# Performance work log

Measured on AMD Instinct MI355X. Metric: run time of the kernel, lower is better.

Reference implementation:

```python
import jax, jax.numpy as jnp
import numpy as np

N = 100000   # num_nodes
E = 600000   # num_edges (before self loops)
H = 128      # hidden_size
R = 16       # lora_rank
SCALING = 32.0 / 16  # lora_alpha / lora_rank
LN_EPS = 1e-5


def setup_inputs() -> dict:
    key = jax.random.key(0)
    ks = jax.random.split(key, 12)
    s = 0.02
    return {
        "hidden_states": jax.random.normal(ks[0], (N, H), dtype=jnp.float32),
        "edge_index": jax.random.randint(ks[1], (2, E), 0, N, dtype=jnp.int64),
        # message_transform (LoRALinear): base W/b + lora A/B
        "msg_W": jax.random.normal(ks[2], (H, H), dtype=jnp.float32) * s,
        "msg_b": jax.random.normal(ks[3], (H,), dtype=jnp.float32) * s,
        "msg_A": jax.random.normal(ks[4], (R, H), dtype=jnp.float32) * s,
        "msg_B": jax.random.normal(ks[5], (H, R), dtype=jnp.float32) * s,
        # gate_transform (LoRALinear)
        "gate_W": jax.random.normal(ks[6], (H, H), dtype=jnp.float32) * s,
        "gate_b": jax.random.normal(ks[7], (H,), dtype=jnp.float32) * s,
        "gate_A": jax.random.normal(ks[8], (R, H), dtype=jnp.float32) * s,
        "gate_B": jax.random.normal(ks[9], (H, R), dtype=jnp.float32) * s,
        # LayerNorm params
        "ln_gamma": jnp.ones((H,), dtype=jnp.float32),
        "ln_beta": jnp.zeros((H,), dtype=jnp.float32),
    }


def _lora_linear(x, W, b, A, B):
    # base_layer(x) + scaling * lora_B(lora_A(x)); dropout is identity at eval
    return x @ W.T + b + SCALING * ((x @ A.T) @ B.T)


def _message_passing(x, edge_index):
    n = x.shape[0]
    loops = jnp.arange(n, dtype=edge_index.dtype)
    row = jnp.concatenate([edge_index[0], loops])  # sources j
    col = jnp.concatenate([edge_index[1], loops])  # targets i
    # symmetric-ish norm: deg from targets (PyG degree(col))
    deg = jax.ops.segment_sum(jnp.ones_like(col, dtype=x.dtype), col, num_segments=n)
    dinv = jnp.where(deg > 0, deg ** -0.5, 0.0)
    norm = dinv[row] * dinv[col]                   # [E+N]
    msgs = norm[:, None] * x[row]                  # edge-gathered messages
    summed = jax.ops.segment_sum(msgs, col, num_segments=n)
    # aggr='mean': divide by per-target edge count (== deg, includes self loop)
    return summed / jnp.maximum(deg, 1.0)[:, None]


def reference(hidden_states, edge_index, msg_W, msg_b, msg_A, msg_B,
              gate_W, gate_b, gate_A, gate_B, ln_gamma, ln_beta):
    message_out = _message_passing(hidden_states, edge_index)
    message_transformed = _lora_linear(message_out, msg_W, msg_b, msg_A, msg_B)
    gate = jax.nn.sigmoid(_lora_linear(hidden_states, gate_W, gate_b, gate_A, gate_B))
    x = hidden_states + gate * message_transformed
    mu = jnp.mean(x, axis=-1, keepdims=True)
    var = jnp.mean(jnp.square(x - mu), axis=-1, keepdims=True)
    return (x - mu) / jnp.sqrt(var + LN_EPS) * ln_gamma + ln_beta
```

## Files before the change

### kernel.cpp

```cpp
#include <hip/hip_runtime.h>
#include <math.h>

#define H 128
#define RANK 16
#define SCALING 2.0f
#define LN_EPS 1e-5f
#define CHUNK 2048

typedef short bf16x8 __attribute__((ext_vector_type(8)));
typedef float f32x4 __attribute__((ext_vector_type(4)));

__device__ __forceinline__ unsigned short f2bf(float f) {
    unsigned int u = __float_as_uint(f);
    u += 0x7fffu + ((u >> 16) & 1u);
    return (unsigned short)(u >> 16);
}
__device__ __forceinline__ float bflo(unsigned int u) {
    return __uint_as_float(u << 16);
}
__device__ __forceinline__ float bfhi(unsigned int u) {
    return __uint_as_float(u & 0xffff0000u);
}

__global__ void k_init(const int* __restrict__ ei, int E, int* __restrict__ deg,
                       const float2* __restrict__ x2, int xtotal, unsigned int* __restrict__ xb,
                       const float* __restrict__ msg_W, const float* __restrict__ msg_A,
                       const float* __restrict__ msg_B,
                       const float* __restrict__ gate_W, const float* __restrict__ gate_A,
                       const float* __restrict__ gate_B,
                       unsigned short* __restrict__ Wmz, unsigned short* __restrict__ Wgz,
                       int BA, int BB) {
    int b = blockIdx.x;
    if (b < BA) {
        int e = b * 256 + threadIdx.x;
        if (e < E) atomicAdd(&deg[ei[E + e]], 1);
    } else if (b < BA + BB) {
        int idx = (b - BA) * 256 + threadIdx.x;
        if (idx < xtotal) {
            float2 v = x2[idx];
            xb[idx] = (unsigned int)f2bf(v.x) | ((unsigned int)f2bf(v.y) << 16);
        }
    } else {
        int bb = b - BA - BB;
        int which = bb >> 6;
        int idx = (bb & 63) * 256 + threadIdx.x;
        const float* W = which ? gate_W : msg_W;
        const float* A = which ? gate_A : msg_A;
        const float* Bm = which ? gate_B : msg_B;
        unsigned short* Wz = which ? Wgz : Wmz;
        int h = idx & (H - 1);
        int k = idx >> 7;
        float s = 0.f;
        #pragma unroll
        for (int r = 0; r < RANK; ++r) s = fmaf(A[r * H + k], Bm[h * RANK + r], s);
        float v = W[h * H + k] + SCALING * s;
        int kt = k >> 5, kk = k & 31, qd = kk >> 3, j = kk & 7;
        int nt = h >> 4, nl = h & 15;
        int lane = qd * 16 + nl;
        Wz[(((kt * 8 + nt) * 64 + lane) * 8) + j] = f2bf(v);
    }
}

__global__ void k_stage2(const int* __restrict__ deg, int N,
                         float* __restrict__ dinv, float* __restrict__ rdeg,
                         int* __restrict__ chunkSum, int BA) {
    int b = blockIdx.x;
    if (b < BA) {
        int i = b * 256 + threadIdx.x;
        if (i < N) {
            float d = (float)(deg[i] + 1);
            dinv[i] = rsqrtf(d);
            rdeg[i] = 1.0f / d;
        }
    } else {
        __shared__ int red[256];
        int c = b - BA;
        int base = c * CHUNK;
        int s = 0;
        for (int i = threadIdx.x; i < CHUNK; i += 256) {
            int g = base + i;
            if (g < N) s += deg[g];
        }
        red[threadIdx.x] = s;
        __syncthreads();
        for (int off = 128; off > 0; off >>= 1) {
            if (threadIdx.x < off) red[threadIdx.x] += red[threadIdx.x + off];
            __syncthreads();
        }
        if (threadIdx.x == 0) chunkSum[c] = red[0];
    }
}

__global__ void k_localscan(const int* __restrict__ deg, int N, const int* __restrict__ chunkSum,
                            int C, int* __restrict__ offsets, int* __restrict__ cursor) {
    int c = blockIdx.x, t = threadIdx.x;
    __shared__ int cbase_sh;
    __shared__ int wsum[4];
    if (t < 64) {
        int partial = 0, total = 0;
        for (int j = t; j < C; j += 64) {
            int v = chunkSum[j];
            total += v;
            if (j < c) partial += v;
        }
        #pragma unroll
        for (int off = 1; off < 64; off <<= 1) {
            partial += __shfl_xor(partial, off);
            total += __shfl_xor(total, off);
        }
        if (t == 0) {
            cbase_sh = partial;
            if (c == C - 1) offsets[N] = total;
        }
    }
    int base = c * CHUNK;
    int idx0 = base + t * 8;
    int v[8]; int tsum = 0;
    #pragma unroll
    for (int j = 0; j < 8; ++j) {
        int g = idx0 + j;
        v[j] = (g < N) ? deg[g] : 0;
        tsum += v[j];
    }
    int lane = t & 63, wv = t >> 6;
    int inc = tsum;
    #pragma unroll
    for (int off = 1; off < 64; off <<= 1) {
        int u = __shfl_up(inc, off);
        if (lane >= off) inc += u;
    }
    if (lane == 63) wsum[wv] = inc;
    __syncthreads();
    int wbase = 0;
    for (int w = 0; w < wv; ++w) wbase += wsum[w];
    int excl = wbase + inc - tsum + cbase_sh;
    #pragma unroll
    for (int j = 0; j < 8; ++j) {
        int g = idx0 + j;
        if (g < N) { offsets[g] = excl; cursor[g] = excl; excl += v[j]; }
    }
}

__global__ void k_fill(const int* __restrict__ ei, int E,
                       int* __restrict__ cursor, int* __restrict__ adj) {
    int e = blockIdx.x * blockDim.x + threadIdx.x;
    if (e < E) {
        int r = ei[e];
        int c = ei[E + e];
        int pos = atomicAdd(&cursor[c], 1);
        adj[pos] = r;
    }
}

__global__ __launch_bounds__(256) void k_gather(
    const unsigned int* __restrict__ xb, const int* __restrict__ offsets,
    const int* __restrict__ adj, const float* __restrict__ dinv,
    const float* __restrict__ rdeg, int N, unsigned int* __restrict__ msgb) {
    int wave = (blockIdx.x * 256 + threadIdx.x) >> 6;
    int lane = threadIdx.x & 63;
    if (wave >= N) return;
    int i = __builtin_amdgcn_readfirstlane(wave);
    float di = dinv[i];
    unsigned int su = xb[(size_t)i * 64 + lane];
    float ax[8], ay[8];
    ax[0] = bflo(su) * di; ay[0] = bfhi(su) * di;
    #pragma unroll
    for (int j = 1; j < 8; ++j) { ax[j] = 0.f; ay[j] = 0.f; }
    int s0 = offsets[i], s1 = offsets[i + 1];
    int last = s1 - 1;
    for (int e = s0; e < s1; e += 8) {
        int is[8]; float ws[8]; unsigned int us[8];
        #pragma unroll
        for (int j = 0; j < 8; ++j) {
            int ee = e + j;
            is[j] = __builtin_amdgcn_readfirstlane(adj[ee < s1 ? ee : last]);
        }
        #pragma unroll
        for (int j = 0; j < 8; ++j) {
            float w = dinv[is[j]];
            ws[j] = (e + j < s1) ? w : 0.f;
        }
        #pragma unroll
        for (int j = 0; j < 8; ++j) us[j] = xb[(size_t)is[j] * 64 + lane];
        #pragma unroll
        for (int j = 0; j < 8; ++j) {
            ax[j] = fmaf(ws[j], bflo(us[j]), ax[j]);
            ay[j] = fmaf(ws[j], bfhi(us[j]), ay[j]);
        }
    }
    float sc = di * rdeg[i];
    float rx = (((ax[0] + ax[1]) + (ax[2] + ax[3])) + ((ax[4] + ax[5]) + (ax[6] + ax[7]))) * sc;
    float ry = (((ay[0] + ay[1]) + (ay[2] + ay[3])) + ((ay[4] + ay[5]) + (ay[6] + ay[7]))) * sc;
    msgb[(size_t)i * 64 + lane] = (unsigned int)f2bf(rx) | ((unsigned int)f2bf(ry) << 16);
}

__global__ __launch_bounds__(256) void k_fused(
    const unsigned int* __restrict__ xb, const unsigned int* __restrict__ msgb,
    const unsigned short* __restrict__ Wmz, const unsigned short* __restrict__ Wgz,
    const float* __restrict__ msg_b, const float* __restrict__ gate_b,
    const float* __restrict__ gamma, const float* __restrict__ beta,
    float* __restrict__ out, int N) {
    int t = threadIdx.x;
    int wid = t >> 6, lane = t & 63;
    int m0 = (blockIdx.x * 4 + wid) * 16;
    if (m0 >= N) return;

    int quad = lane >> 4;
    int nl = lane & 15;

    int arow = m0 + nl; if (arow >= N) arow = N - 1;
    const bf16x8* hb8 = (const bf16x8*)xb + (size_t)arow * 16;
    const bf16x8* mb8 = (const bf16x8*)msgb + (size_t)arow * 16;

    f32x4 accg[8], accm[8];
    #pragma unroll
    for (int nt = 0; nt < 8; ++nt) {
        accg[nt] = (f32x4)(0.f);
        accm[nt] = (f32x4)(0.f);
    }

    #pragma unroll
    for (int kt = 0; kt < 4; ++kt) {
        bf16x8 ah = hb8[kt * 4 + quad];
        bf16x8 am = mb8[kt * 4 + quad];
        const bf16x8* bg8 = (const bf16x8*)(Wgz + (size_t)kt * 4096);
        const bf16x8* bm8 = (const bf16x8*)(Wmz + (size_t)kt * 4096);
        #pragma unroll
        for (int nt = 0; nt < 8; ++nt) {
            bf16x8 bg = bg8[nt * 64 + lane];
            bf16x8 bm = bm8[nt * 64 + lane];
            accg[nt] = __builtin_amdgcn_mfma_f32_16x16x32_bf16(ah, bg, accg[nt], 0, 0, 0);
            accm[nt] = __builtin_amdgcn_mfma_f32_16x16x32_bf16(am, bm, accm[nt], 0, 0, 0);
        }
    }

    float gb[8], mb[8], gm[8], bt[8];
    #pragma unroll
    for (int nt = 0; nt < 8; ++nt) {
        int col = nt * 16 + nl;
        gb[nt] = gate_b[col]; mb[nt] = msg_b[col];
        gm[nt] = gamma[col];  bt[nt] = beta[col];
    }

    const unsigned short* xs = (const unsigned short*)xb;

    #pragma unroll
    for (int r = 0; r < 4; ++r) {
        int node = m0 + quad * 4 + r;
        int hnode = node < N ? node : N - 1;
        const unsigned short* hrow = xs + (size_t)hnode * H;
        float xr[8]; float s = 0.f, ss = 0.f;
        #pragma unroll
        for (int nt = 0; nt < 8; ++nt) {
            int col = nt * 16 + nl;
            float hv = __uint_as_float((unsigned int)hrow[col] << 16);
            float g = 1.f / (1.f + __expf(-(accg[nt][r] + gb[nt])));
            float m = accm[nt][r] + mb[nt];
            float v = fmaf(g, m, hv);
            xr[nt] = v; s += v; ss = fmaf(v, v, ss);
        }
        #pragma unroll
        for (int msk = 1; msk < 16; msk <<= 1) {
            s += __shfl_xor(s, msk);
            ss += __shfl_xor(ss, msk);
        }
        float mu = s * (1.f / 128.f);
        float var = ss * (1.f / 128.f) - mu * mu;
        float rstd = rsqrtf(var + LN_EPS);
        if (node < N) {
            float* orow = out + (size_t)node * H;
            #pragma unroll
            for (int nt = 0; nt < 8; ++nt)
                orow[nt * 16 + nl] = (xr[nt] - mu) * rstd * gm[nt] + bt[nt];
        }
    }
}

extern "C" void kernel_launch(void* const* d_in, const int* in_sizes, int n_in,
                              void* d_out, int out_size, void* d_ws, size_t ws_size,
                              hipStream_t stream) {
    const float* hidden = (const float*)d_in[0];
    const int*   ei     = (const int*)d_in[1];
    const float* msg_W  = (const float*)d_in[2];
    const float* msg_b  = (const float*)d_in[3];
    const float* msg_A  = (const float*)d_in[4];
    const float* msg_B  = (const float*)d_in[5];
    const float* gate_W = (const float*)d_in[6];
    const float* gate_b = (const float*)d_in[7];
    const float* gate_A = (const float*)d_in[8];
    const float* gate_B = (const float*)d_in[9];
    const float* gamma  = (const float*)d_in[10];
    const float* beta   = (const float*)d_in[11];
    float* out = (float*)d_out;

    int N = in_sizes[0] / H;
    int E = in_sizes[1] / 2;
    int C = (N + CHUNK - 1) / CHUNK;

    char* p = (char*)d_ws;
    unsigned short* Wmz = (unsigned short*)p;  p += (size_t)H * H * sizeof(unsigned short);
    unsigned short* Wgz = (unsigned short*)p;  p += (size_t)H * H * sizeof(unsigned short);
    float* dinv = (float*)p;               p += (size_t)N * sizeof(float);
    float* rdeg = (float*)p;               p += (size_t)N * sizeof(float);
    int*   deg  = (int*)p;                 p += (size_t)N * sizeof(int);
    int*   offsets = (int*)p;              p += (size_t)(N + 1) * sizeof(int);
    int*   cursor  = (int*)p;              p += (size_t)N * sizeof(int);
    int*   chunkSum  = (int*)p;            p += (size_t)C * sizeof(int);
    int*   adj  = (int*)p;                 p += (size_t)E * sizeof(int);
    unsigned int* xb   = (unsigned int*)p; p += (size_t)N * 64 * sizeof(unsigned int);
    unsigned int* msgb = (unsigned int*)p; p += (size_t)N * 64 * sizeof(unsigned int);

    hipMemsetAsync(deg, 0, (size_t)N * sizeof(int), stream);

    int xtotal = N * 64;
    int BA = (E + 255) / 256;
    int BB = (xtotal + 255) / 256;
    k_init<<<BA + BB + 128, 256, 0, stream>>>(
        ei, E, deg, (const float2*)hidden, xtotal, xb,
        msg_W, msg_A, msg_B, gate_W, gate_A, gate_B, Wmz, Wgz, BA, BB);

    int BD = (N + 255) / 256;
    k_stage2<<<BD + C, 256, 0, stream>>>(deg, N, dinv, rdeg, chunkSum, BD);

    k_localscan<<<C, 256, 0, stream>>>(deg, N, chunkSum, C, offsets, cursor);
    k_fill<<<(E + 255) / 256, 256, 0, stream>>>(ei, E, cursor, adj);
    k_gather<<<((size_t)N * 64 + 255) / 256, 256, 0, stream>>>(
        xb, offsets, adj, dinv, rdeg, N, msgb);
    int waves = (N + 15) / 16;
    k_fused<<<(waves + 3) / 4, 256, 0, stream>>>(
        xb, msgb, Wmz, Wgz, msg_b, gate_b, gamma, beta, out, N);
}
```

Measured before the change: 265.3 us.

## Build CSR with per-chunk shared-memory histograms and fused scan-fill

Replaces the global-atomic degree count, separate stage2/localscan/fill kernels and the memset with two kernels. Each block owns a 2048-node chunk and one of four edge slices, counts degrees with shared-memory atomics, and writes per-slice partial counts. A second kernel scans these counts, computes dinv/rdeg, and fills the adjacency using shared-memory cursors. The bf16 conversion of x is widened to 16 floats per thread. Every block now scans its whole edge slice, so edge-index reads grow by roughly the number of chunks, in exchange for fewer launches and no global atomics.

Measured after the change: 344.9 us. +30.0%, slower.

```diff
diff --git a/kernel.cpp b/kernel.cpp
--- a/kernel.cpp
+++ b/kernel.cpp
@@ -6,6 +6,7 @@
 #define SCALING 2.0f
 #define LN_EPS 1e-5f
 #define CHUNK 2048
+#define NSLICE 4
 
 typedef short bf16x8 __attribute__((ext_vector_type(8)));
 typedef float f32x4 __attribute__((ext_vector_type(4)));
@@ -15,6 +16,9 @@
     u += 0x7fffu + ((u >> 16) & 1u);
     return (unsigned short)(u >> 16);
 }
+__device__ __forceinline__ unsigned int pk2(float a, float b) {
+    return (unsigned int)f2bf(a) | ((unsigned int)f2bf(b) << 16);
+}
 __device__ __forceinline__ float bflo(unsigned int u) {
     return __uint_as_float(u << 16);
 }
@@ -22,28 +26,67 @@
     return __uint_as_float(u & 0xffff0000u);
 }
 
-__global__ void k_init(const int* __restrict__ ei, int E, int* __restrict__ deg,
-                       const float2* __restrict__ x2, int xtotal, unsigned int* __restrict__ xb,
-                       const float* __restrict__ msg_W, const float* __restrict__ msg_A,
-                       const float* __restrict__ msg_B,
-                       const float* __restrict__ gate_W, const float* __restrict__ gate_A,
-                       const float* __restrict__ gate_B,
-                       unsigned short* __restrict__ Wmz, unsigned short* __restrict__ Wgz,
-                       int BA, int BB) {
+__global__ __launch_bounds__(256) void k_prep(
+    const int* __restrict__ ei, int E, int N,
+    int* __restrict__ part,
+    int* __restrict__ pcs,
+    const float4* __restrict__ x4, int total16, unsigned int* __restrict__ xb,
+    const float* __restrict__ msg_W, const float* __restrict__ msg_A,
+    const float* __restrict__ msg_B,
+    const float* __restrict__ gate_W, const float* __restrict__ gate_A,
+    const float* __restrict__ gate_B,
+    unsigned short* __restrict__ Wmz, unsigned short* __restrict__ Wgz,
+    int BH) {
+    __shared__ int sh[CHUNK];
+    __shared__ int shred[4];
     int b = blockIdx.x;
-    if (b < BA) {
-        int e = b * 256 + threadIdx.x;
-        if (e < E) atomicAdd(&deg[ei[E + e]], 1);
-    } else if (b < BA + BB) {
-        int idx = (b - BA) * 256 + threadIdx.x;
-        if (idx < xtotal) {
-            float2 v = x2[idx];
-            xb[idx] = (unsigned int)f2bf(v.x) | ((unsigned int)f2bf(v.y) << 16);
-        }
-    } else {
-        int bb = b - BA - BB;
+    int t = threadIdx.x;
+    if (b < BH) {
+        int c = b >> 2, s = b & 3;
+        int base = c * CHUNK;
+        for (int i = t; i < CHUNK; i += 256) sh[i] = 0;
+        __syncthreads();
+        int Es = ((E + NSLICE - 1) / NSLICE + 3) & ~3;
+        int es = s * Es, ee = min(E, es + Es);
+        const int* col = ei + E;
+        if (es < ee) {
+            if ((E & 3) == 0) {
+                const int4* colv = (const int4*)col;
+                for (int q = (es >> 2) + t; (q << 2) < ee; q += 256) {
+                    int4 v = colv[q];
+                    int e0 = q << 2;
+                    int vv[4] = {v.x, v.y, v.z, v.w};
+                    #pragma unroll
+                    for (int j = 0; j < 4; ++j) {
+                        unsigned int rel = (unsigned int)(vv[j] - base);
+                        if (e0 + j < ee && rel < CHUNK) atomicAdd(&sh[rel], 1);
+                    }
+                }
+            } else {
+                for (int e = es + t; e < ee; e += 256) {
+                    unsigned int rel = (unsigned int)(col[e] - base);
+                    if (rel < CHUNK) atomicAdd(&sh[rel], 1);
+                }
+            }
+        }
+        __syncthreads();
+        int bsum = 0;
+        for (int i = t; i < CHUNK; i += 256) {
+            int v = sh[i];
+            int g = base + i;
+            if (g < N) part[(size_t)s * N + g] = v;
+            bsum += v;
+        }
+        #pragma unroll
+        for (int off = 1; off < 64; off <<= 1) bsum += __shfl_xor(bsum, off);
+        int lane = t & 63, wv = t >> 6;
+        if (lane == 0) shred[wv] = bsum;
+        __syncthreads();
+        if (t == 0) pcs[c * NSLICE + s] = shred[0] + shred[1] + shred[2] + shred[3];
+    } else if (b < BH + 128) {
+        int bb = b - BH;
         int which = bb >> 6;
-        int idx = (bb & 63) * 256 + threadIdx.x;
+        int idx = (bb & 63) * 256 + t;
         const float* W = which ? gate_W : msg_W;
         const float* A = which ? gate_A : msg_A;
         const float* Bm = which ? gate_B : msg_B;
@@ -58,50 +101,43 @@
         int nt = h >> 4, nl = h & 15;
         int lane = qd * 16 + nl;
         Wz[(((kt * 8 + nt) * 64 + lane) * 8) + j] = f2bf(v);
-    }
-}
-
-__global__ void k_stage2(const int* __restrict__ deg, int N,
-                         float* __restrict__ dinv, float* __restrict__ rdeg,
-                         int* __restrict__ chunkSum, int BA) {
+    } else {
+        int idx = (b - BH - 128) * 256 + t;
+        if (idx < total16) {
+            float4 a = x4[idx * 4 + 0];
+            float4 bq = x4[idx * 4 + 1];
+            float4 cq = x4[idx * 4 + 2];
+            float4 dq = x4[idx * 4 + 3];
+            uint4 o0, o1;
+            o0.x = pk2(a.x, a.y);  o0.y = pk2(a.z, a.w);
+            o0.z = pk2(bq.x, bq.y); o0.w = pk2(bq.z, bq.w);
+            o1.x = pk2(cq.x, cq.y); o1.y = pk2(cq.z, cq.w);
+            o1.z = pk2(dq.x, dq.y); o1.w = pk2(dq.z, dq.w);
+            uint4* xb4 = (uint4*)xb;
+            xb4[idx * 2 + 0] = o0;
+            xb4[idx * 2 + 1] = o1;
+        }
+    }
+}
+
+__global__ __launch_bounds__(256) void k_scanfill(
+    const int* __restrict__ ei, int E, int N, int C,
+    const int* __restrict__ part, const int* __restrict__ pcs,
+    int* __restrict__ offsets, float* __restrict__ dinv, float* __restrict__ rdeg,
+    int* __restrict__ adj) {
+    __shared__ int cur[CHUNK];
+    __shared__ int wsum[4];
+    __shared__ int cbase_sh;
     int b = blockIdx.x;
-    if (b < BA) {
-        int i = b * 256 + threadIdx.x;
-        if (i < N) {
-            float d = (float)(deg[i] + 1);
-            dinv[i] = rsqrtf(d);
-            rdeg[i] = 1.0f / d;
-        }
-    } else {
-        __shared__ int red[256];
-        int c = b - BA;
-        int base = c * CHUNK;
-        int s = 0;
-        for (int i = threadIdx.x; i < CHUNK; i += 256) {
-            int g = base + i;
-            if (g < N) s += deg[g];
-        }
-        red[threadIdx.x] = s;
-        __syncthreads();
-        for (int off = 128; off > 0; off >>= 1) {
-            if (threadIdx.x < off) red[threadIdx.x] += red[threadIdx.x + off];
-            __syncthreads();
-        }
-        if (threadIdx.x == 0) chunkSum[c] = red[0];
-    }
-}
-
-__global__ void k_localscan(const int* __restrict__ deg, int N, const int* __restrict__ chunkSum,
-                            int C, int* __restrict__ offsets, int* __restrict__ cursor) {
-    int c = blockIdx.x, t = threadIdx.x;
-    __shared__ int cbase_sh;
-    __shared__ int wsum[4];
+    int c = b >> 2, s = b & 3;
+    int t = threadIdx.x;
+
     if (t < 64) {
         int partial = 0, total = 0;
-        for (int j = t; j < C; j += 64) {
-            int v = chunkSum[j];
+        for (int j = t; j < C * NSLICE; j += 64) {
+            int v = pcs[j];
             total += v;
-            if (j < c) partial += v;
+            if ((j >> 2) < c) partial += v;
         }
         #pragma unroll
         for (int off = 1; off < 64; off <<= 1) {
@@ -110,18 +146,29 @@
         }
         if (t == 0) {
             cbase_sh = partial;
-            if (c == C - 1) offsets[N] = total;
-        }
-    }
+            if (c == C - 1 && s == 0) offsets[N] = total;
+        }
+    }
+
     int base = c * CHUNK;
     int idx0 = base + t * 8;
-    int v[8]; int tsum = 0;
-    #pragma unroll
-    for (int j = 0; j < 8; ++j) {
-        int g = idx0 + j;
-        v[j] = (g < N) ? deg[g] : 0;
-        tsum += v[j];
-    }
+    int d8[8], pre8[8];
+    #pragma unroll
+    for (int j = 0; j < 8; ++j) { d8[j] = 0; pre8[j] = 0; }
+    for (int ss = 0; ss < NSLICE; ++ss) {
+        const int* p = part + (size_t)ss * N;
+        #pragma unroll
+        for (int j = 0; j < 8; ++j) {
+            int g = idx0 + j;
+            int v = (g < N) ? p[g] : 0;
+            d8[j] += v;
+            if (ss < s) pre8[j] += v;
+        }
+    }
+    int tsum = 0;
+    #pragma unroll
+    for (int j = 0; j < 8; ++j) tsum += d8[j];
+
     int lane = t & 63, wv = t >> 6;
     int inc = tsum;
     #pragma unroll
@@ -137,18 +184,47 @@
     #pragma unroll
     for (int j = 0; j < 8; ++j) {
         int g = idx0 + j;
-        if (g < N) { offsets[g] = excl; cursor[g] = excl; excl += v[j]; }
-    }
-}
-
-__global__ void k_fill(const int* __restrict__ ei, int E,
-                       int* __restrict__ cursor, int* __restrict__ adj) {
-    int e = blockIdx.x * blockDim.x + threadIdx.x;
-    if (e < E) {
-        int r = ei[e];
-        int c = ei[E + e];
-        int pos = atomicAdd(&cursor[c], 1);
-        adj[pos] = r;
+        if (g < N) {
+            cur[t * 8 + j] = excl + pre8[j];
+            if (s == 0) {
+                offsets[g] = excl;
+                float dd = (float)(d8[j] + 1);
+                dinv[g] = rsqrtf(dd);
+                rdeg[g] = 1.0f / dd;
+            }
+            excl += d8[j];
+        }
+    }
+    __syncthreads();
+
+    int Es = ((E + NSLICE - 1) / NSLICE + 3) & ~3;
+    int es = s * Es, ee = min(E, es + Es);
+    const int* col = ei + E;
+    if (es < ee) {
+        if ((E & 3) == 0) {
+            const int4* colv = (const int4*)col;
+            for (int q = (es >> 2) + t; (q << 2) < ee; q += 256) {
+                int4 v = colv[q];
+                int e0 = q << 2;
+                int vv[4] = {v.x, v.y, v.z, v.w};
+                #pragma unroll
+                for (int j = 0; j < 4; ++j) {
+                    unsigned int rel = (unsigned int)(vv[j] - base);
+                    if (e0 + j < ee && rel < CHUNK) {
+                        int pos = atomicAdd(&cur[rel], 1);
+                        adj[pos] = ei[e0 + j];
+                    }
+                }
+            }
+        } else {
+            for (int e = es + t; e < ee; e += 256) {
+                unsigned int rel = (unsigned int)(col[e] - base);
+                if (rel < CHUNK) {
+                    int pos = atomicAdd(&cur[rel], 1);
+                    adj[pos] = ei[e];
+                }
+            }
+        }
     }
 }
 
@@ -296,36 +372,33 @@
     int N = in_sizes[0] / H;
     int E = in_sizes[1] / 2;
     int C = (N + CHUNK - 1) / CHUNK;
+    int BH = C * NSLICE;
 
     char* p = (char*)d_ws;
     unsigned short* Wmz = (unsigned short*)p;  p += (size_t)H * H * sizeof(unsigned short);
     unsigned short* Wgz = (unsigned short*)p;  p += (size_t)H * H * sizeof(unsigned short);
-    float* dinv = (float*)p;               p += (size_t)N * sizeof(float);
-    float* rdeg = (float*)p;               p += (size_t)N * sizeof(float);
-    int*   deg  = (int*)p;                 p += (size_t)N * sizeof(int);
-    int*   offsets = (int*)p;              p += (size_t)(N + 1) * sizeof(int);
-    int*   cursor  = (int*)p;              p += (size_t)N * sizeof(int);
-    int*   chunkSum  = (int*)p;            p += (size_t)C * sizeof(int);
-    int*   adj  = (int*)p;                 p += (size_t)E * sizeof(int);
-    unsigned int* xb   = (unsigned int*)p; p += (size_t)N * 64 * sizeof(unsigned int);
-    unsigned int* msgb = (unsigned int*)p; p += (size_t)N * 64 * sizeof(unsigned int);
-
-    hipMemsetAsync(deg, 0, (size_t)N * sizeof(int), stream);
-
-    int xtotal = N * 64;
-    int BA = (E + 255) / 256;
-    int BB = (xtotal + 255) / 256;
-    k_init<<<BA + BB + 128, 256, 0, stream>>>(
-        ei, E, deg, (const float2*)hidden, xtotal, xb,
-        msg_W, msg_A, msg_B, gate_W, gate_A, gate_B, Wmz, Wgz, BA, BB);
-
-    int BD = (N + 255) / 256;
-    k_stage2<<<BD + C, 256, 0, stream>>>(deg, N, dinv, rdeg, chunkSum, BD);
-
-    k_localscan<<<C, 256, 0, stream>>>(deg, N, chunkSum, C, offsets, cursor);
-    k_fill<<<(E + 255) / 256, 256, 0, stream>>>(ei, E, cursor, adj);
+    unsigned int* xb   = (unsigned int*)p;     p += (size_t)N * 64 * sizeof(unsigned int);
+    unsigned int* msgb = (unsigned int*)p;     p += (size_t)N * 64 * sizeof(unsigned int);
+    int*   part = (int*)p;                     p += (size_t)NSLICE * N * sizeof(int);
+    float* dinv = (float*)p;                   p += (size_t)N * sizeof(float);
+    float* rdeg = (float*)p;                   p += (size_t)N * sizeof(float);
+    int*   offsets = (int*)p;                  p += (size_t)(N + 1) * sizeof(int);
+    int*   pcs  = (int*)p;                     p += (size_t)BH * sizeof(int);
+    int*   adj  = (int*)p;                     p += (size_t)E * sizeof(int);
+
+    int total16 = (N * H) >> 4;
+    int BB = (total16 + 255) / 256;
+
+    k_prep<<<BH + 128 + BB, 256, 0, stream>>>(
+        ei, E, N, part, pcs, (const float4*)hidden, total16, xb,
+        msg_W, msg_A, msg_B, gate_W, gate_A, gate_B, Wmz, Wgz, BH);
+
+    k_scanfill<<<BH, 256, 0, stream>>>(
+        ei, E, N, C, part, pcs, offsets, dinv, rdeg, adj);
+
     k_gather<<<((size_t)N * 64 + 255) / 256, 256, 0, stream>>>(
         xb, offsets, adj, dinv, rdeg, N, msgb);
+
     int waves = (N + 15) / 16;
     k_fused<<<(waves + 3) / 4, 256, 0, stream>>>(
         xb, msgb, Wmz, Wgz, msg_b, gate_b, gamma, beta, out, N);
```
